# Kernel tuning notes

Hardware: AMD Instinct MI355X
Metric: run time of the kernel (lower is better)

The kernel has to match this reference:

```python
import jax, jax.numpy as jnp
import numpy as np

B, T, D_MODEL = 4, 8192, 1024
D_K, D_V = 128, 128
DILATIONS = [1, 2, 4, 8]
SEG = 128                      # segment_count for every head
NORM = 1.0 / np.sqrt(D_K)      # norm_fact = 1/sqrt(d_k)
H = len(DILATIONS)


def setup_inputs() -> dict:
    key = jax.random.key(0)
    ks = jax.random.split(key, 6)
    x = jax.random.normal(ks[0], (B, T, D_MODEL), dtype=jnp.float32)
    # head weights, init like torch: randn(k, m)/sqrt(k), stacked over heads
    Wk = jax.random.normal(ks[1], (H, D_K, D_MODEL), dtype=jnp.float32) / np.sqrt(D_K)
    Wq = jax.random.normal(ks[2], (H, D_K, D_MODEL), dtype=jnp.float32) / np.sqrt(D_K)
    Wv = jax.random.normal(ks[3], (H, D_V, D_MODEL), dtype=jnp.float32) / np.sqrt(D_V)
    # output projection (concat of H heads -> d_model), torch Linear layout (out, in)
    W_out = jax.random.normal(ks[4], (D_MODEL, H * D_V), dtype=jnp.float32) / np.sqrt(H * D_V)
    b_out = jnp.zeros((D_MODEL,), dtype=jnp.float32)
    return {"x": x, "Wk": Wk, "Wq": Wq, "Wv": Wv, "W_out": W_out, "b_out": b_out}


def _head(x, wk, wq, wv, dil):
    """SingleHeadDilatedSelfAttention with padding='same', is_causal=True."""
    Bb, Tt, E = x.shape
    nb = Tt // SEG                       # attention length before dilation
    # view(B, T//seg, seg, E).permute(0,2,3,1) -> (B, seg, E, nb); dilate last dim
    xv = x.reshape(Bb, nb, SEG, E).transpose(0, 2, 3, 1)[:, :, :, ::dil]  # (B, seg, E, L)
    Q = jnp.einsum('bsel,ke->bslk', xv, wq)   # (B, seg, L, d_k)
    K = jnp.einsum('bsel,ke->bslk', xv, wk)
    V = jnp.einsum('bsel,ve->bslv', xv, wv)   # (B, seg, L, d_v)
    # KQ[b,s,n,m]: n = key position, m = query position
    KQ = jnp.einsum('bsnd,bsmd->bsnm', K, Q)
    mask = jnp.tril(jnp.ones((nb, nb), dtype=bool))[::dil, ::dil]  # (L, L)
    KQ = jnp.where(mask, KQ, -jnp.inf)
    # original applies softmax along dim 3 (the query axis) of KQ * norm_fact
    smKQ = jax.nn.softmax(KQ * NORM, axis=3)
    att = jnp.einsum('bsnm,bsnv->bsmv', smKQ, V)   # (B, seg, L, d_v)
    L = att.shape[2]
    # 'same' padding: strided scatter back to full sequence length
    out = jnp.zeros((Bb, Tt, D_V), dtype=x.dtype)
    out = out.at[:, ::dil, :].set(att.reshape(Bb, SEG * L, D_V))
    return out


def reference(x, Wk, Wq, Wv, W_out, b_out):
    heads = [_head(x, Wk[h], Wq[h], Wv[h], DILATIONS[h]) for h in range(H)]
    cat = jnp.concatenate(heads, axis=-1)            # (B, T, H*d_v)
    return cat @ W_out.T + b_out                     # (B, T, d_model)
```

## Files before the change

### kernel.cpp

```cpp
#include <hip/hip_runtime.h>
#include <cstdint>
#include <cstddef>

typedef __attribute__((ext_vector_type(8))) short bf16x8;
typedef __attribute__((ext_vector_type(4))) float f32x4;

__device__ __forceinline__ unsigned short f2bf(float f) {
  union { float f; uint32_t u; } v; v.f = f;
  uint32_t r = v.u + 0x7fffu + ((v.u >> 16) & 1u);
  return (unsigned short)(r >> 16);
}
__device__ __forceinline__ float bf2f(unsigned short u) {
  union { uint32_t u; float f; } v; v.u = ((uint32_t)u) << 16;
  return v.f;
}

__device__ __forceinline__ size_t head_off(int h) {
  return (size_t)65536 * ((h == 0) ? 0 : (h == 1) ? 64 : (h == 2) ? 96 : 112);
}

__global__ void k_cvt(const float* __restrict__ src, unsigned short* __restrict__ dst, int n4) {
  int i = blockIdx.x * 256 + threadIdx.x;
  if (i < n4) {
    float4 f = ((const float4*)src)[i];
    ushort4 u;
    u.x = f2bf(f.x); u.y = f2bf(f.y); u.z = f2bf(f.z); u.w = f2bf(f.w);
    ((ushort4*)dst)[i] = u;
  }
}

__global__ void k_cvt_w(const float* __restrict__ Wq, const float* __restrict__ Wk,
                        const float* __restrict__ Wv, unsigned short* __restrict__ dst) {
  int row = blockIdx.x;
  int h = row / 384, j = row % 384;
  const float* src = (j < 128) ? (Wq + (size_t)(h * 128 + j) * 1024)
                   : (j < 256) ? (Wk + (size_t)(h * 128 + j - 128) * 1024)
                               : (Wv + (size_t)(h * 128 + j - 256) * 1024);
  int e = threadIdx.x * 4;
  float4 f = *(const float4*)(src + e);
  ushort4 u;
  u.x = f2bf(f.x); u.y = f2bf(f.y); u.z = f2bf(f.z); u.w = f2bf(f.w);
  *(ushort4*)(dst + (size_t)row * 1024 + e) = u;
}

__global__ __launch_bounds__(256) void k_qkv(
    const unsigned short* __restrict__ xbf,
    const unsigned short* __restrict__ wbf,
    unsigned short* __restrict__ qws,
    unsigned short* __restrict__ kws,
    unsigned short* __restrict__ vws) {
  int gx = blockIdx.x, gy = blockIdx.y;
  int h, base;
  if (gx < 256)      { h = 0; base = 0; }
  else if (gx < 384) { h = 1; base = 256; }
  else if (gx < 448) { h = 2; base = 384; }
  else               { h = 3; base = 448; }
  int L = 64 >> h, dil = 1 << h;
  int inner = gx - base;
  int b = inner >> (6 - h);
  int l = inner & (L - 1);
  const unsigned short* Abase = xbf + ((size_t)(b * 8192 + l * dil * 128)) * 1024;
  const unsigned short* Bbase = wbf + ((size_t)(h * 384 + gy * 128)) * 1024;

  __shared__ unsigned short As[128][72];
  __shared__ unsigned short Bs[128][72];

  int tid = threadIdx.x;
  int lane = tid & 63, wave = tid >> 6;
  int wm = wave >> 1, wn = wave & 1;
  int li = lane & 15, lk8 = (lane >> 4) << 3;

  f32x4 acc[4][4] = {};

  int sr = tid >> 1, sc = (tid & 1) * 32;
  const unsigned short* Ag = Abase + (size_t)sr * 1024 + sc;
  const unsigned short* Bg = Bbase + (size_t)sr * 1024 + sc;

  for (int kc = 0; kc < 1024; kc += 64) {
    bf16x8 av[4], bv[4];
#pragma unroll
    for (int i = 0; i < 4; ++i) {
      av[i] = *(const bf16x8*)(Ag + kc + i * 8);
      bv[i] = *(const bf16x8*)(Bg + kc + i * 8);
    }
    __syncthreads();
#pragma unroll
    for (int i = 0; i < 4; ++i) {
      *(bf16x8*)&As[sr][sc + i * 8] = av[i];
      *(bf16x8*)&Bs[sr][sc + i * 8] = bv[i];
    }
    __syncthreads();
#pragma unroll
    for (int kk = 0; kk < 2; ++kk) {
      int k0 = kk * 32 + lk8;
      bf16x8 af[4], bfv[4];
#pragma unroll
      for (int mf = 0; mf < 4; ++mf)
        af[mf] = *(const bf16x8*)&As[wm * 64 + mf * 16 + li][k0];
#pragma unroll
      for (int nf = 0; nf < 4; ++nf)
        bfv[nf] = *(const bf16x8*)&Bs[wn * 64 + nf * 16 + li][k0];
#pragma unroll
      for (int mf = 0; mf < 4; ++mf)
#pragma unroll
        for (int nf = 0; nf < 4; ++nf)
          acc[mf][nf] = __builtin_amdgcn_mfma_f32_16x16x32_bf16(af[mf], bfv[nf], acc[mf][nf], 0, 0, 0);
    }
  }
  unsigned short* dst = ((gy == 0) ? qws : (gy == 1) ? kws : vws) + head_off(h);
  int ib = (lane >> 4) * 4;
#pragma unroll
  for (int mf = 0; mf < 4; ++mf) {
#pragma unroll
    for (int nf = 0; nf < 4; ++nf) {
#pragma unroll
      for (int rg = 0; rg < 4; ++rg) {
        int s = wm * 64 + mf * 16 + ib + rg;
        int j = wn * 64 + nf * 16 + li;
        dst[((size_t)((b * 128 + s) * L + l)) * 128 + j] = f2bf(acc[mf][nf][rg]);
      }
    }
  }
}

__global__ __launch_bounds__(256) void k_attn(
    const unsigned short* __restrict__ qws,
    const unsigned short* __restrict__ kws,
    const unsigned short* __restrict__ vws,
    unsigned short* __restrict__ att) {
  int bx = blockIdx.x;
  int h, inst;
  if (bx < 512)      { h = 0; inst = bx; }
  else if (bx < 768) { h = 1; inst = bx - 512; }
  else if (bx < 896) { h = 2; inst = bx - 768; }
  else               { h = 3; inst = bx - 896; }
  int lgL = 6 - h;
  int L = 64 >> h;
  int Lm1 = L - 1;
  int bpb = 128 >> h;
  int b = inst / bpb;
  int s0 = (inst % bpb) << h;
  size_t off0 = head_off(h) + ((size_t)(b * 128 + s0) * L) * 128;
  const unsigned short* Qg = qws + off0;
  const unsigned short* Kg = kws + off0;
  const unsigned short* Vg = vws + off0;
  unsigned short* Og = att + off0;

  __shared__ unsigned short PT[64][72];
  __shared__ unsigned short VtL[128][72];

  int tid = threadIdx.x;
  int lane = tid & 63, w = tid >> 6;
  int li = lane & 15, q = lane >> 4;
  int lk8 = q << 3;

#pragma unroll
  for (int c = 0; c < 4; ++c) {
    int u = tid + c * 256;
    int n = u & 63, vblk = u >> 6;
    bf16x8 ve = *(const bf16x8*)(Vg + n * 128 + vblk * 8);
#pragma unroll
    for (int j = 0; j < 8; ++j)
      VtL[vblk * 8 + j][n] = (unsigned short)ve[j];
  }

  f32x4 sacc[4] = {};
  int nrow = 16 * w + li;
  for (int kc = 0; kc < 4; ++kc) {
    int d0 = kc * 32 + lk8;
    bf16x8 af = *(const bf16x8*)(Kg + nrow * 128 + d0);
#pragma unroll
    for (int mt = 0; mt < 4; ++mt) {
      bf16x8 bfq = *(const bf16x8*)(Qg + (mt * 16 + li) * 128 + d0);
      sacc[mt] = __builtin_amdgcn_mfma_f32_16x16x32_bf16(af, bfq, sacc[mt], 0, 0, 0);
    }
  }

  float sv[4][4];
#pragma unroll
  for (int mt = 0; mt < 4; ++mt)
#pragma unroll
    for (int r = 0; r < 4; ++r) {
      int n = 16 * w + 4 * q + r;
      int m = mt * 16 + li;
      bool valid = ((m >> lgL) == (n >> lgL)) && ((m & Lm1) <= (n & Lm1));
      sv[mt][r] = valid ? sacc[mt][r] * 0.08838834764831845f : -1e30f;
    }
  float inv[4];
#pragma unroll
  for (int r = 0; r < 4; ++r) {
    float m0 = fmaxf(fmaxf(sv[0][r], sv[1][r]), fmaxf(sv[2][r], sv[3][r]));
#pragma unroll
    for (int d = 1; d < 16; d <<= 1)
      m0 = fmaxf(m0, __shfl_xor(m0, d, 64));
    float s0 = 0.f;
#pragma unroll
    for (int mt = 0; mt < 4; ++mt) {
      sv[mt][r] = __expf(sv[mt][r] - m0);
      s0 += sv[mt][r];
    }
#pragma unroll
    for (int d = 1; d < 16; d <<= 1)
      s0 += __shfl_xor(s0, d, 64);
    inv[r] = 1.f / s0;
  }

#pragma unroll
  for (int mt = 0; mt < 4; ++mt) {
    ushort4 pk;
    pk.x = f2bf(sv[mt][0] * inv[0]);
    pk.y = f2bf(sv[mt][1] * inv[1]);
    pk.z = f2bf(sv[mt][2] * inv[2]);
    pk.w = f2bf(sv[mt][3] * inv[3]);
    *(ushort4*)&PT[mt * 16 + li][16 * w + 4 * q] = pk;
  }
  __syncthreads();

  f32x4 oacc[8] = {};
#pragma unroll
  for (int ks = 0; ks < 2; ++ks) {
    int n0 = ks * 32 + lk8;
    bf16x8 af = *(const bf16x8*)&PT[16 * w + li][n0];
#pragma unroll
    for (int vt = 0; vt < 8; ++vt) {
      bf16x8 bfv = *(const bf16x8*)&VtL[vt * 16 + li][n0];
      oacc[vt] = __builtin_amdgcn_mfma_f32_16x16x32_bf16(af, bfv, oacc[vt], 0, 0, 0);
    }
  }
#pragma unroll
  for (int vt = 0; vt < 8; ++vt) {
#pragma unroll
    for (int r = 0; r < 4; ++r) {
      int m = 16 * w + 4 * q + r;
      int v = vt * 16 + li;
      Og[m * 128 + v] = f2bf(oacc[vt][r]);
    }
  }
}

__global__ __launch_bounds__(256) void k_out(
    const unsigned short* __restrict__ att,
    const unsigned short* __restrict__ wout,
    const float* __restrict__ bout,
    float* __restrict__ out) {
  int mt = blockIdx.x, nt = blockIdx.y;
  int row0 = mt * 128;

  __shared__ unsigned short As[128][72];
  __shared__ unsigned short Bs[128][72];

  int tid = threadIdx.x;
  int lane = tid & 63, wave = tid >> 6;
  int wm = wave >> 1, wn = wave & 1;
  int li = lane & 15, lk8 = (lane >> 4) << 3;

  f32x4 acc[4][4] = {};

  int sr = tid >> 1, sc = (tid & 1) * 32;
  int rowg = row0 + sr;
  int b = rowg >> 13, t = rowg & 8191;
  const unsigned short* Bg = wout + (size_t)(nt * 128 + sr) * 512 + sc;
  const bf16x8 ZV = {0, 0, 0, 0, 0, 0, 0, 0};

  for (int kc = 0; kc < 512; kc += 64) {
    int c0 = kc + sc;
    int hd = c0 >> 7, v0 = c0 & 127;
    int dil = 1 << hd, Lh = 64 >> hd;
    bf16x8 av[4], bv[4];
    if ((t & (dil - 1)) == 0) {
      int j = t >> hd;
      int s = j >> (6 - hd), l = j & (Lh - 1);
      const unsigned short* Ag = att + head_off(hd)
          + ((size_t)((b * 128 + s) * Lh + l)) * 128 + v0;
#pragma unroll
      for (int i = 0; i < 4; ++i) av[i] = *(const bf16x8*)(Ag + i * 8);
    } else {
#pragma unroll
      for (int i = 0; i < 4; ++i) av[i] = ZV;
    }
#pragma unroll
    for (int i = 0; i < 4; ++i) bv[i] = *(const bf16x8*)(Bg + kc + i * 8);
    __syncthreads();
#pragma unroll
    for (int i = 0; i < 4; ++i) {
      *(bf16x8*)&As[sr][sc + i * 8] = av[i];
      *(bf16x8*)&Bs[sr][sc + i * 8] = bv[i];
    }
    __syncthreads();
#pragma unroll
    for (int kk = 0; kk < 2; ++kk) {
      int k0 = kk * 32 + lk8;
      bf16x8 af[4], bfv[4];
#pragma unroll
      for (int mf = 0; mf < 4; ++mf)
        af[mf] = *(const bf16x8*)&As[wm * 64 + mf * 16 + li][k0];
#pragma unroll
      for (int nf = 0; nf < 4; ++nf)
        bfv[nf] = *(const bf16x8*)&Bs[wn * 64 + nf * 16 + li][k0];
#pragma unroll
      for (int mf = 0; mf < 4; ++mf)
#pragma unroll
        for (int nf = 0; nf < 4; ++nf)
          acc[mf][nf] = __builtin_amdgcn_mfma_f32_16x16x32_bf16(af[mf], bfv[nf], acc[mf][nf], 0, 0, 0);
    }
  }
  int ib = (lane >> 4) * 4;
#pragma unroll
  for (int mf = 0; mf < 4; ++mf) {
#pragma unroll
    for (int nf = 0; nf < 4; ++nf) {
      int col = nt * 128 + wn * 64 + nf * 16 + li;
      float bo = bout[col];
#pragma unroll
      for (int rg = 0; rg < 4; ++rg) {
        int r = row0 + wm * 64 + mf * 16 + ib + rg;
        out[(size_t)r * 1024 + col] = acc[mf][nf][rg] + bo;
      }
    }
  }
}

extern "C" void kernel_launch(void* const* d_in, const int* in_sizes, int n_in,
                              void* d_out, int out_size, void* d_ws, size_t ws_size,
                              hipStream_t stream) {
  const float* x  = (const float*)d_in[0];
  const float* Wk = (const float*)d_in[1];
  const float* Wq = (const float*)d_in[2];
  const float* Wv = (const float*)d_in[3];
  const float* Wo = (const float*)d_in[4];
  const float* bo = (const float*)d_in[5];
  float* out = (float*)d_out;
  char* ws = (char*)d_ws;
  unsigned short* xbf  = (unsigned short*)(ws);
  unsigned short* wbf  = (unsigned short*)(ws + 67108864);
  unsigned short* wobf = (unsigned short*)(ws + 70254592);
  unsigned short* qws  = (unsigned short*)(ws + 71303168);
  unsigned short* kws  = (unsigned short*)(ws + 87031808);
  unsigned short* vws  = (unsigned short*)(ws + 102760448);
  unsigned short* attw = (unsigned short*)(ws + 118489088);

  k_cvt<<<dim3(32768), dim3(256), 0, stream>>>(x, xbf, 8388608);
  k_cvt_w<<<dim3(1536), dim3(256), 0, stream>>>(Wq, Wk, Wv, wbf);
  k_cvt<<<dim3(512), dim3(256), 0, stream>>>(Wo, wobf, 131072);
  k_qkv<<<dim3(480, 3), dim3(256), 0, stream>>>(xbf, wbf, qws, kws, vws);
  k_attn<<<dim3(960), dim3(256), 0, stream>>>(qws, kws, vws, attw);
  k_out<<<dim3(256, 8), dim3(256), 0, stream>>>(attw, wobf, bo, out);
}
```

Before: 372.3 us.

## Use direct global-to-LDS loads in GEMMs and remap QKV grid for L2 reuse

The QKV and output-projection GEMMs now stage tiles with global_load_lds, which writes 16-byte chunks from global memory straight into shared memory instead of passing them through registers. The shared tiles lose their padding and become dense 64-wide rows. The QKV grid is flattened and remapped so the three Q/K/V blocks of each group of 8 x-tiles run close together, aiming for L2 reuse of x. In exchange the unpadded LDS layout may cause bank conflicts on the fragment reads, and the loads are still not double-buffered.

```diff
diff --git a/kernel.cpp b/kernel.cpp
--- a/kernel.cpp
+++ b/kernel.cpp
@@ -13,6 +13,12 @@
 __device__ __forceinline__ float bf2f(unsigned short u) {
   union { uint32_t u; float f; } v; v.u = ((uint32_t)u) << 16;
   return v.f;
+}
+
+__device__ __forceinline__ void glds16(const void* g, void* l) {
+  __builtin_amdgcn_global_load_lds(
+      (const __attribute__((address_space(1))) unsigned int*)g,
+      (__attribute__((address_space(3))) unsigned int*)l, 16, 0, 0);
 }
 
 __device__ __forceinline__ size_t head_off(int h) {
@@ -49,7 +55,10 @@
     unsigned short* __restrict__ qws,
     unsigned short* __restrict__ kws,
     unsigned short* __restrict__ vws) {
-  int gx = blockIdx.x, gy = blockIdx.y;
+  int i = blockIdx.x;
+  int group = i / 24, jj = i - group * 24;
+  int gy = jj >> 3, slot = jj & 7;
+  int gx = group * 8 + slot;
   int h, base;
   if (gx < 256)      { h = 0; base = 0; }
   else if (gx < 384) { h = 1; base = 256; }
@@ -62,32 +71,26 @@
   const unsigned short* Abase = xbf + ((size_t)(b * 8192 + l * dil * 128)) * 1024;
   const unsigned short* Bbase = wbf + ((size_t)(h * 384 + gy * 128)) * 1024;
 
-  __shared__ unsigned short As[128][72];
-  __shared__ unsigned short Bs[128][72];
+  __shared__ unsigned short As[128 * 64];
+  __shared__ unsigned short Bs[128 * 64];
 
   int tid = threadIdx.x;
   int lane = tid & 63, wave = tid >> 6;
   int wm = wave >> 1, wn = wave & 1;
   int li = lane & 15, lk8 = (lane >> 4) << 3;
 
+  int urow = tid >> 3;
+  int uc8 = (tid & 7) << 3;
+
   f32x4 acc[4][4] = {};
 
-  int sr = tid >> 1, sc = (tid & 1) * 32;
-  const unsigned short* Ag = Abase + (size_t)sr * 1024 + sc;
-  const unsigned short* Bg = Bbase + (size_t)sr * 1024 + sc;
-
   for (int kc = 0; kc < 1024; kc += 64) {
-    bf16x8 av[4], bv[4];
-#pragma unroll
-    for (int i = 0; i < 4; ++i) {
-      av[i] = *(const bf16x8*)(Ag + kc + i * 8);
-      bv[i] = *(const bf16x8*)(Bg + kc + i * 8);
-    }
     __syncthreads();
 #pragma unroll
-    for (int i = 0; i < 4; ++i) {
-      *(bf16x8*)&As[sr][sc + i * 8] = av[i];
-      *(bf16x8*)&Bs[sr][sc + i * 8] = bv[i];
+    for (int it = 0; it < 4; ++it) {
+      int row = it * 32 + urow;
+      glds16(Abase + (size_t)row * 1024 + kc + uc8, &As[it * 2048 + wave * 512]);
+      glds16(Bbase + (size_t)row * 1024 + kc + uc8, &Bs[it * 2048 + wave * 512]);
     }
     __syncthreads();
 #pragma unroll
@@ -96,10 +99,10 @@
       bf16x8 af[4], bfv[4];
 #pragma unroll
       for (int mf = 0; mf < 4; ++mf)
-        af[mf] = *(const bf16x8*)&As[wm * 64 + mf * 16 + li][k0];
+        af[mf] = *(const bf16x8*)&As[(wm * 64 + mf * 16 + li) * 64 + k0];
 #pragma unroll
       for (int nf = 0; nf < 4; ++nf)
-        bfv[nf] = *(const bf16x8*)&Bs[wn * 64 + nf * 16 + li][k0];
+        bfv[nf] = *(const bf16x8*)&Bs[(wn * 64 + nf * 16 + li) * 64 + k0];
 #pragma unroll
       for (int mf = 0; mf < 4; ++mf)
 #pragma unroll
@@ -246,45 +249,42 @@
   int mt = blockIdx.x, nt = blockIdx.y;
   int row0 = mt * 128;
 
-  __shared__ unsigned short As[128][72];
-  __shared__ unsigned short Bs[128][72];
+  __shared__ unsigned short As[128 * 64];
+  __shared__ unsigned short Bs[128 * 64];
 
   int tid = threadIdx.x;
   int lane = tid & 63, wave = tid >> 6;
   int wm = wave >> 1, wn = wave & 1;
   int li = lane & 15, lk8 = (lane >> 4) << 3;
 
+  int urow = tid >> 3;
+  int uc8 = (tid & 7) << 3;
+  const bf16x8 ZV = {0, 0, 0, 0, 0, 0, 0, 0};
+
   f32x4 acc[4][4] = {};
 
-  int sr = tid >> 1, sc = (tid & 1) * 32;
-  int rowg = row0 + sr;
-  int b = rowg >> 13, t = rowg & 8191;
-  const unsigned short* Bg = wout + (size_t)(nt * 128 + sr) * 512 + sc;
-  const bf16x8 ZV = {0, 0, 0, 0, 0, 0, 0, 0};
-
   for (int kc = 0; kc < 512; kc += 64) {
-    int c0 = kc + sc;
-    int hd = c0 >> 7, v0 = c0 & 127;
-    int dil = 1 << hd, Lh = 64 >> hd;
-    bf16x8 av[4], bv[4];
-    if ((t & (dil - 1)) == 0) {
-      int j = t >> hd;
-      int s = j >> (6 - hd), l = j & (Lh - 1);
-      const unsigned short* Ag = att + head_off(hd)
-          + ((size_t)((b * 128 + s) * Lh + l)) * 128 + v0;
-#pragma unroll
-      for (int i = 0; i < 4; ++i) av[i] = *(const bf16x8*)(Ag + i * 8);
-    } else {
-#pragma unroll
-      for (int i = 0; i < 4; ++i) av[i] = ZV;
-    }
-#pragma unroll
-    for (int i = 0; i < 4; ++i) bv[i] = *(const bf16x8*)(Bg + kc + i * 8);
+    int hd = kc >> 7;
+    int dil = 1 << hd, Lh = 64 >> hd, v0 = kc & 127;
     __syncthreads();
 #pragma unroll
-    for (int i = 0; i < 4; ++i) {
-      *(bf16x8*)&As[sr][sc + i * 8] = av[i];
-      *(bf16x8*)&Bs[sr][sc + i * 8] = bv[i];
+    for (int it = 0; it < 4; ++it) {
+      int row = it * 32 + urow;
+      glds16(wout + (size_t)(nt * 128 + row) * 512 + kc + uc8, &Bs[it * 2048 + wave * 512]);
+    }
+#pragma unroll
+    for (int it = 0; it < 4; ++it) {
+      int row = it * 32 + urow;
+      int rg = row0 + row;
+      int b = rg >> 13, t = rg & 8191;
+      if ((t & (dil - 1)) == 0) {
+        int j2 = t >> hd;
+        int s = j2 >> (6 - hd), l2 = j2 & (Lh - 1);
+        glds16(att + head_off(hd) + ((size_t)((b * 128 + s) * Lh + l2)) * 128 + v0 + uc8,
+               &As[it * 2048 + wave * 512]);
+      } else {
+        *(bf16x8*)&As[it * 2048 + wave * 512 + lane * 8] = ZV;
+      }
     }
     __syncthreads();
 #pragma unroll
@@ -293,10 +293,10 @@
       bf16x8 af[4], bfv[4];
 #pragma unroll
       for (int mf = 0; mf < 4; ++mf)
-        af[mf] = *(const bf16x8*)&As[wm * 64 + mf * 16 + li][k0];
+        af[mf] = *(const bf16x8*)&As[(wm * 64 + mf * 16 + li) * 64 + k0];
 #pragma unroll
       for (int nf = 0; nf < 4; ++nf)
-        bfv[nf] = *(const bf16x8*)&Bs[wn * 64 + nf * 16 + li][k0];
+        bfv[nf] = *(const bf16x8*)&Bs[(wn * 64 + nf * 16 + li) * 64 + k0];
 #pragma unroll
       for (int mf = 0; mf < 4; ++mf)
 #pragma unroll
@@ -342,7 +342,7 @@
   k_cvt<<<dim3(32768), dim3(256), 0, stream>>>(x, xbf, 8388608);
   k_cvt_w<<<dim3(1536), dim3(256), 0, stream>>>(Wq, Wk, Wv, wbf);
   k_cvt<<<dim3(512), dim3(256), 0, stream>>>(Wo, wobf, 131072);
-  k_qkv<<<dim3(480, 3), dim3(256), 0, stream>>>(xbf, wbf, qws, kws, vws);
+  k_qkv<<<dim3(1440), dim3(256), 0, stream>>>(xbf, wbf, qws, kws, vws);
   k_attn<<<dim3(960), dim3(256), 0, stream>>>(qws, kws, vws, attw);
   k_out<<<dim3(256, 8), dim3(256), 0, stream>>>(attw, wobf, bo, out);
 }
```

Measured after the change: 375.3 us. Within noise of the previous version (+0.8%).
